# Kernel tuning notes

Measured on AMD Instinct MI355X. Metric: run time of the kernel, lower is better.

The kernel has to match this reference:

```python
import jax, jax.numpy as jnp
import numpy as np

# Grid constants from PolarVoxelizer defaults
Z_MIN = -2.0
Z_STEP = 0.2
Z_DEPTH = 100            # round((18 - (-2)) / 0.2)
FOV = 2.268
NUM_A = 192
NUM_R = 320
R_MIN = 2.7
R_MAX = 165.0


def setup_inputs() -> dict:
    key = jax.random.key(0)
    k1, k2 = jax.random.split(key)
    B, S, N = 2, 3, 250000
    # x,y spread over the scene; z within [z_min, z_max) so floor() stays in range
    xy = jax.random.normal(k1, (B, S, N, 2), dtype=jnp.float32) * 40.0
    z = jax.random.uniform(k2, (B, S, N, 1), dtype=jnp.float32, minval=-2.0, maxval=17.99)
    lidars = jnp.concatenate([xy, z], axis=-1)  # [B,S,N,3]
    # angle bins: linspace(-fov/2, fov/2, 192)
    angle_bins = jnp.linspace(-FOV / 2, FOV / 2, NUM_A, dtype=jnp.float32)
    # log-spaced radius bins, force_num_r_bins=True branch
    kmax = NUM_R - 1
    delta = ((R_MAX + 0.0001) / R_MIN) ** (1.0 / kmax) - 1.0
    r_bins = (R_MIN * (1.0 + delta) ** jnp.arange(NUM_R, dtype=jnp.float32)).astype(jnp.float32)
    return {"lidars": lidars, "r_bins": r_bins, "angle_bins": angle_bins}


def reference(lidars, r_bins, angle_bins):
    B, S, N, _ = lidars.shape
    x, y, z = lidars[..., 0], lidars[..., 1], lidars[..., 2]
    angles = jnp.arctan2(y, x)                       # [B,S,N]
    radius = jnp.sqrt(x * x + y * y)                 # [B,S,N]
    mask = (jnp.abs(angles) < FOV / 2) & (radius < R_MAX) & (radius > R_MIN)
    # torch.bucketize(right=False) == searchsorted side='left'
    xg = jnp.searchsorted(r_bins, radius, side='left').astype(jnp.int32)
    yg = jnp.searchsorted(angle_bins, angles, side='left').astype(jnp.int32)
    zg = jnp.floor((z - Z_MIN) / Z_STEP).astype(jnp.int32)
    # linear index into flat bev [B,S,Z,A,R]; masked-out points -> OOB, dropped
    bs = (jnp.arange(B, dtype=jnp.int32)[:, None] * S
          + jnp.arange(S, dtype=jnp.int32)[None, :])[:, :, None]  # [B,S,1]
    lin = ((bs * Z_DEPTH + zg) * NUM_A + yg) * NUM_R + xg
    total = B * S * Z_DEPTH * NUM_A * NUM_R
    lin = jnp.where(mask, lin, total)
    bev = jnp.zeros((total,), dtype=jnp.float32).at[lin.ravel()].set(1.0, mode='drop')
    # original returns bev.view(B, S*Z, A, R)[0]
    return bev.reshape(B, S * Z_DEPTH, NUM_A, NUM_R)[0]
```

## Files before the change

kernel.cpp:

```cpp
#include <hip/hip_runtime.h>

constexpr int Z_DEPTH = 100;
constexpr int NUM_A   = 192;
constexpr int NUM_R   = 320;
constexpr int S_SWEEP = 3;
constexpr int A_CELLS = S_SWEEP * Z_DEPTH * NUM_A * NUM_R;

__global__ __launch_bounds__(256)
void polar_voxelize_kernel(const float* __restrict__ lidars,
                           const float* __restrict__ r_bins,
                           const float* __restrict__ angle_bins,
                           float* __restrict__ out,
                           int n_per_sweep, int out_total)
{
#pragma clang fp contract(off)
    __shared__ float s_r[NUM_R];
    __shared__ float s_a[NUM_A];
    for (int i = threadIdx.x; i < NUM_R; i += blockDim.x) s_r[i] = r_bins[i];
    for (int i = threadIdx.x; i < NUM_A; i += blockDim.x) s_a[i] = angle_bins[i];
    __syncthreads();

    const int s    = blockIdx.y;
    const int tid  = blockIdx.x * blockDim.x + threadIdx.x;
    const int base = tid * 4;

    auto compute_points = [&]() {
        if (base >= n_per_sweep) return;
        const float* sw = lidars + (size_t)s * n_per_sweep * 3;
        float px[4], py[4], pz[4];
        int npt;
        if (base + 4 <= n_per_sweep) {
            npt = 4;
            const float4* v = (const float4*)(sw + (size_t)base * 3);
            float4 a = v[0], b = v[1], c = v[2];
            px[0] = a.x; py[0] = a.y; pz[0] = a.z;
            px[1] = a.w; py[1] = b.x; pz[1] = b.y;
            px[2] = b.z; py[2] = b.w; pz[2] = c.x;
            px[3] = c.y; py[3] = c.z; pz[3] = c.w;
        } else {
            npt = n_per_sweep - base;
            for (int j = 0; j < npt; ++j) {
                px[j] = sw[(size_t)(base + j) * 3 + 0];
                py[j] = sw[(size_t)(base + j) * 3 + 1];
                pz[j] = sw[(size_t)(base + j) * 3 + 2];
            }
        }

        const float fov_half = (float)(2.268 * 0.5);
#pragma unroll
        for (int j = 0; j < 4; ++j) {
            if (j >= npt) break;
            float x = px[j], y = py[j], z = pz[j];

            float xx = x * x;
            float yy = y * y;
            float rr = xx + yy;
            float radius = sqrtf(rr);

            float ang = (float)atan2((double)y, (double)x);

            if (!(fabsf(ang) < fov_half && radius < 165.0f && radius > 2.7f)) continue;

            int lo = 0, hi = NUM_R;
            while (lo < hi) { int m = (lo + hi) >> 1; if (s_r[m] < radius) lo = m + 1; else hi = m; }
            int xg = lo;
            lo = 0; hi = NUM_A;
            while (lo < hi) { int m = (lo + hi) >> 1; if (s_a[m] < ang) lo = m + 1; else hi = m; }
            int yg = lo;

            int zg = (int)floorf((z - (-2.0f)) / 0.2f);

            int lin = ((s * Z_DEPTH + zg) * NUM_A + yg) * NUM_R + xg;
            out[lin] = 1.0f;
        }
    };

    auto zero_region_b = [&]() {
        if (out_total <= A_CELLS) return;
        float4* dst = (float4*)(out + A_CELLS);
        const int nvec = (out_total - A_CELLS) >> 2;
        const int gid  = (blockIdx.y * gridDim.x + blockIdx.x) * blockDim.x + threadIdx.x;
        const int gsz  = gridDim.x * gridDim.y * blockDim.x;
        const float4 z4 = make_float4(0.f, 0.f, 0.f, 0.f);
        for (int i = gid; i < nvec; i += gsz) dst[i] = z4;
        for (int i = A_CELLS + (nvec << 2) + gid; i < out_total; i += gsz) out[i] = 0.f;
    };

    if ((blockIdx.x ^ blockIdx.y) & 1) { zero_region_b(); compute_points(); }
    else                               { compute_points(); zero_region_b(); }
}

extern "C" void kernel_launch(void* const* d_in, const int* in_sizes, int n_in,
                              void* d_out, int out_size, void* d_ws, size_t ws_size,
                              hipStream_t stream)
{
    const float* lidars     = (const float*)d_in[0];
    const float* r_bins     = (const float*)d_in[1];
    const float* angle_bins = (const float*)d_in[2];
    float* out = (float*)d_out;

    const int B = 2;
    int total_pts   = in_sizes[0] / 3;
    int n_per_sweep = total_pts / (B * S_SWEEP);

    int a_cells = out_size < A_CELLS ? out_size : A_CELLS;
    hipMemsetAsync(d_out, 0, (size_t)a_cells * sizeof(float), stream);

    int threads_per_sweep = (n_per_sweep + 3) / 4;
    dim3 block(256);
    dim3 grid((threads_per_sweep + 255) / 256, S_SWEEP);
    polar_voxelize_kernel<<<grid, block, 0, stream>>>(lidars, r_bins, angle_bins,
                                                      out, n_per_sweep, out_size);
}
```

Before: 101.0 us.

## Split voxelization into compute-to-workspace and scatter kernels with in-kernel zeroing

Instead of a memset for the first batch region followed by a kernel that computes indices and scatters, the first kernel now computes linear indices into a workspace while also zeroing the first region in-kernel. A second kernel then performs the scatter of 1.0 values and zeroes the second batch region. This removes the separate memset and overlaps the index math with the zero fill, at the cost of an extra launch and a round trip through the workspace. It falls back to memset plus direct scatter when the workspace is too small.

After: 100.4 us. About the same (-0.6%).

```diff
diff --git a/kernel.cpp b/kernel.cpp
--- a/kernel.cpp
+++ b/kernel.cpp
@@ -6,12 +6,14 @@
 constexpr int S_SWEEP = 3;
 constexpr int A_CELLS = S_SWEEP * Z_DEPTH * NUM_A * NUM_R;
 
+template<bool DIRECT>
 __global__ __launch_bounds__(256)
-void polar_voxelize_kernel(const float* __restrict__ lidars,
-                           const float* __restrict__ r_bins,
-                           const float* __restrict__ angle_bins,
-                           float* __restrict__ out,
-                           int n_per_sweep, int out_total)
+void polar_compute_kernel(const float* __restrict__ lidars,
+                          const float* __restrict__ r_bins,
+                          const float* __restrict__ angle_bins,
+                          float* __restrict__ out,
+                          int* __restrict__ ws,
+                          int n_per_sweep, int tpw)
 {
 #pragma clang fp contract(off)
     __shared__ float s_r[NUM_R];
@@ -47,6 +49,7 @@
         }
 
         const float fov_half = (float)(2.268 * 0.5);
+        int lin4[4] = {-1, -1, -1, -1};
 #pragma unroll
         for (int j = 0; j < 4; ++j) {
             if (j >= npt) break;
@@ -71,23 +74,53 @@
             int zg = (int)floorf((z - (-2.0f)) / 0.2f);
 
             int lin = ((s * Z_DEPTH + zg) * NUM_A + yg) * NUM_R + xg;
-            out[lin] = 1.0f;
+            if (DIRECT) out[lin] = 1.0f;
+            else        lin4[j] = lin;
+        }
+        if (!DIRECT) {
+            *(int4*)(ws + ((size_t)s * tpw + tid) * 4) =
+                make_int4(lin4[0], lin4[1], lin4[2], lin4[3]);
         }
     };
 
-    auto zero_region_b = [&]() {
-        if (out_total <= A_CELLS) return;
-        float4* dst = (float4*)(out + A_CELLS);
-        const int nvec = (out_total - A_CELLS) >> 2;
+    auto zero_a = [&]() {
+        if (DIRECT) return;
+        float4* dst = (float4*)out;
+        const int nvec = A_CELLS >> 2;
         const int gid  = (blockIdx.y * gridDim.x + blockIdx.x) * blockDim.x + threadIdx.x;
         const int gsz  = gridDim.x * gridDim.y * blockDim.x;
         const float4 z4 = make_float4(0.f, 0.f, 0.f, 0.f);
         for (int i = gid; i < nvec; i += gsz) dst[i] = z4;
-        for (int i = A_CELLS + (nvec << 2) + gid; i < out_total; i += gsz) out[i] = 0.f;
     };
 
-    if ((blockIdx.x ^ blockIdx.y) & 1) { zero_region_b(); compute_points(); }
-    else                               { compute_points(); zero_region_b(); }
+    if ((blockIdx.x ^ blockIdx.y) & 1) { zero_a(); compute_points(); }
+    else                               { compute_points(); zero_a(); }
+}
+
+__global__ __launch_bounds__(256)
+void scatter_and_zeroB_kernel(float* __restrict__ out,
+                              const int* __restrict__ ws,
+                              int nslot4, int out_total)
+{
+    const int gid = blockIdx.x * blockDim.x + threadIdx.x;
+    const int gsz = gridDim.x * blockDim.x;
+
+    const int4* w4 = (const int4*)ws;
+    for (int i = gid; i < nslot4; i += gsz) {
+        int4 l = w4[i];
+        if (l.x >= 0) out[l.x] = 1.0f;
+        if (l.y >= 0) out[l.y] = 1.0f;
+        if (l.z >= 0) out[l.z] = 1.0f;
+        if (l.w >= 0) out[l.w] = 1.0f;
+    }
+
+    if (out_total > A_CELLS) {
+        float4* dst = (float4*)(out + A_CELLS);
+        const int nvec = (out_total - A_CELLS) >> 2;
+        const float4 z4 = make_float4(0.f, 0.f, 0.f, 0.f);
+        for (int i = gid; i < nvec; i += gsz) dst[i] = z4;
+        for (int i = A_CELLS + (nvec << 2) + gid; i < out_total; i += gsz) out[i] = 0.f;
+    }
 }
 
 extern "C" void kernel_launch(void* const* d_in, const int* in_sizes, int n_in,
@@ -102,13 +135,22 @@
     const int B = 2;
     int total_pts   = in_sizes[0] / 3;
     int n_per_sweep = total_pts / (B * S_SWEEP);
+    int tpw         = (n_per_sweep + 3) / 4;
 
-    int a_cells = out_size < A_CELLS ? out_size : A_CELLS;
-    hipMemsetAsync(d_out, 0, (size_t)a_cells * sizeof(float), stream);
+    size_t ws_need = (size_t)S_SWEEP * tpw * 4 * sizeof(int);
+    dim3 block(256);
+    dim3 grid((tpw + 255) / 256, S_SWEEP);
 
-    int threads_per_sweep = (n_per_sweep + 3) / 4;
-    dim3 block(256);
-    dim3 grid((threads_per_sweep + 255) / 256, S_SWEEP);
-    polar_voxelize_kernel<<<grid, block, 0, stream>>>(lidars, r_bins, angle_bins,
-                                                      out, n_per_sweep, out_size);
+    if (ws_size >= ws_need && out_size >= A_CELLS) {
+        polar_compute_kernel<false><<<grid, block, 0, stream>>>(
+            lidars, r_bins, angle_bins, out, (int*)d_ws, n_per_sweep, tpw);
+        int nslot4 = S_SWEEP * tpw;
+        dim3 g2(2048);
+        scatter_and_zeroB_kernel<<<g2, block, 0, stream>>>(
+            out, (const int*)d_ws, nslot4, out_size);
+    } else {
+        hipMemsetAsync(d_out, 0, (size_t)out_size * sizeof(float), stream);
+        polar_compute_kernel<true><<<grid, block, 0, stream>>>(
+            lidars, r_bins, angle_bins, out, nullptr, n_per_sweep, tpw);
+    }
 }
```
